# Kernel tuning notes

Hardware: AMD Instinct MI355X
Metric: run time of the kernel (lower is better)

## Reference

```python
import jax, jax.numpy as jnp
import numpy as np

B, L, C, R = 64, 4096, 256, 8
H = C // R  # 32

def setup_inputs() -> dict:
    key = jax.random.key(0)
    k0, k1, k2 = jax.random.split(key, 3)
    inputs = jax.random.normal(k0, (B, L, C), dtype=jnp.float32)
    # Dense weights (glorot-ish scale)
    w1 = jax.random.normal(k1, (C, H), dtype=jnp.float32) * (1.0 / np.sqrt(C))
    b1 = jnp.zeros((H,), dtype=jnp.float32)
    w2 = jax.random.normal(k2, (H, C), dtype=jnp.float32) * (1.0 / np.sqrt(H))
    b2 = jnp.zeros((C,), dtype=jnp.float32)
    return {"inputs": inputs, "w1": w1, "b1": b1, "w2": w2, "b2": b2}

def reference(inputs, w1, b1, w2, b2):
    # squeeze: global average pool over sequence dim -> [B, C]
    s = jnp.mean(inputs, axis=1)
    # excitation: C -> C//R (relu) -> C (sigmoid)
    e = jax.nn.relu(s @ w1 + b1)
    g = jax.nn.sigmoid(e @ w2 + b2)  # [B, C]
    # broadcast gate over sequence dim and scale
    return inputs * g[:, None, :]
```

## Files before the change

kernel.cpp:

```cpp
#include <hip/hip_runtime.h>
#include <math.h>

constexpr int B = 64;
constexpr int L = 4096;
constexpr int C = 256;
constexpr int H = 32;

constexpr int NCHUNK = 32;
constexpr int ROWS = L / NCHUNK;

typedef float v4f __attribute__((ext_vector_type(4)));

__global__ __launch_bounds__(256) void se_reduce(const float* __restrict__ in,
                                                 float* __restrict__ partial) {
    const int b = blockIdx.x / NCHUNK;
    const int chunk = blockIdx.x % NCHUNK;
    const int t = threadIdx.x;
    const int c4 = t & 63;
    const int r0 = t >> 6;

    const v4f* base = reinterpret_cast<const v4f*>(
        in + (size_t)b * L * C + (size_t)chunk * ROWS * C);

    v4f acc = (v4f)(0.f);
    for (int r = r0; r < ROWS; r += 4) {
        acc += base[(size_t)r * (C / 4) + c4];
    }

    __shared__ v4f red[4][C / 4];
    red[r0][c4] = acc;
    __syncthreads();
    if (r0 == 0) {
        v4f s = red[0][c4] + red[1][c4] + red[2][c4] + red[3][c4];
        reinterpret_cast<v4f*>(partial + (size_t)blockIdx.x * C)[c4] = s;
    }
}

__global__ __launch_bounds__(256) void se_gate(const float* __restrict__ partial,
                                               const float* __restrict__ w1,
                                               const float* __restrict__ b1,
                                               const float* __restrict__ w2,
                                               const float* __restrict__ b2,
                                               float* __restrict__ g) {
    const int b = blockIdx.x;
    const int t = threadIdx.x;

    __shared__ float sm[C];
    __shared__ float em[H];

    float acc = 0.f;
    const float* p = partial + (size_t)b * NCHUNK * C + t;
    #pragma unroll 8
    for (int k = 0; k < NCHUNK; ++k) acc += p[(size_t)k * C];
    sm[t] = acc * (1.0f / (float)L);
    __syncthreads();

    if (t < H) {
        float a1 = b1[t];
        #pragma unroll 8
        for (int c = 0; c < C; ++c) a1 += sm[c] * w1[c * H + t];
        em[t] = fmaxf(a1, 0.0f);
    }
    __syncthreads();

    float a2 = b2[t];
    #pragma unroll
    for (int h = 0; h < H; ++h) a2 += em[h] * w2[h * C + t];
    g[b * C + t] = 1.0f / (1.0f + expf(-a2));
}

constexpr size_t TOT4 = (size_t)B * L * C / 4;
constexpr int SCALE_BLOCKS = 2048;
constexpr int SCALE_THREADS = 256;

__global__ __launch_bounds__(256) void se_scale(const v4f* __restrict__ in,
                                                const float* __restrict__ g,
                                                v4f* __restrict__ out) {
    const size_t stride = (size_t)SCALE_BLOCKS * SCALE_THREADS;
    const size_t nsteps = TOT4 / stride;
    const size_t tid = (size_t)blockIdx.x * SCALE_THREADS + threadIdx.x;
    const v4f* g4 = reinterpret_cast<const v4f*>(g);

    for (size_t k = nsteps; k-- > 0;) {
        const size_t i = k * stride + tid;
        v4f v = in[i];
        const size_t b = i >> 18;
        const int c4 = (int)(i & (C / 4 - 1));
        const v4f gv = g4[b * (C / 4) + c4];
        v *= gv;
        __builtin_nontemporal_store(v, &out[i]);
    }
}

extern "C" void kernel_launch(void* const* d_in, const int* in_sizes, int n_in,
                              void* d_out, int out_size, void* d_ws, size_t ws_size,
                              hipStream_t stream) {
    const float* in = (const float*)d_in[0];
    const float* w1 = (const float*)d_in[1];
    const float* b1 = (const float*)d_in[2];
    const float* w2 = (const float*)d_in[3];
    const float* b2 = (const float*)d_in[4];
    float* out = (float*)d_out;

    float* partial = (float*)d_ws;
    float* g = partial + (size_t)B * NCHUNK * C;

    se_reduce<<<B * NCHUNK, 256, 0, stream>>>(in, partial);
    se_gate<<<B, 256, 0, stream>>>(partial, w1, b1, w2, b2, g);
    se_scale<<<SCALE_BLOCKS, SCALE_THREADS, 0, stream>>>(
        reinterpret_cast<const v4f*>(in), g, reinterpret_cast<v4f*>(out));
}
```

Measured before the change: 147.9 us.

## Segment batch into two passes so scale rereads input from cache

Splits the reduce, gate and scale pipeline into two batch segments, launching all three kernels per segment. Each segment's input is small enough that the scale pass can re-read it from the last-level cache right after the reduce pass streamed it, instead of going back to HBM. The scale kernel is also rewritten to use the same chunked block mapping as reduce, with loop unrolling added. This adds extra kernel launches and serialization of the small gate kernel between segments.

```diff
diff --git a/kernel.cpp b/kernel.cpp
--- a/kernel.cpp
+++ b/kernel.cpp
@@ -6,15 +6,18 @@
 constexpr int C = 256;
 constexpr int H = 32;
 
-constexpr int NCHUNK = 32;
-constexpr int ROWS = L / NCHUNK;
+constexpr int NSEG = 2;
+constexpr int BSEG = B / NSEG;
+constexpr int NCH = 32;
+constexpr int ROWS = L / NCH;
 
 typedef float v4f __attribute__((ext_vector_type(4)));
 
 __global__ __launch_bounds__(256) void se_reduce(const float* __restrict__ in,
-                                                 float* __restrict__ partial) {
-    const int b = blockIdx.x / NCHUNK;
-    const int chunk = blockIdx.x % NCHUNK;
+                                                 float* __restrict__ partial,
+                                                 int b0) {
+    const int b = b0 + blockIdx.x / NCH;
+    const int chunk = blockIdx.x % NCH;
     const int t = threadIdx.x;
     const int c4 = t & 63;
     const int r0 = t >> 6;
@@ -23,6 +26,7 @@
         in + (size_t)b * L * C + (size_t)chunk * ROWS * C);
 
     v4f acc = (v4f)(0.f);
+    #pragma unroll 8
     for (int r = r0; r < ROWS; r += 4) {
         acc += base[(size_t)r * (C / 4) + c4];
     }
@@ -32,7 +36,7 @@
     __syncthreads();
     if (r0 == 0) {
         v4f s = red[0][c4] + red[1][c4] + red[2][c4] + red[3][c4];
-        reinterpret_cast<v4f*>(partial + (size_t)blockIdx.x * C)[c4] = s;
+        reinterpret_cast<v4f*>(partial + ((size_t)b * NCH + chunk) * C)[c4] = s;
     }
 }
 
@@ -41,17 +45,18 @@
                                                const float* __restrict__ b1,
                                                const float* __restrict__ w2,
                                                const float* __restrict__ b2,
-                                               float* __restrict__ g) {
-    const int b = blockIdx.x;
+                                               float* __restrict__ g,
+                                               int b0) {
+    const int b = b0 + blockIdx.x;
     const int t = threadIdx.x;
 
     __shared__ float sm[C];
     __shared__ float em[H];
 
     float acc = 0.f;
-    const float* p = partial + (size_t)b * NCHUNK * C + t;
+    const float* p = partial + (size_t)b * NCH * C + t;
     #pragma unroll 8
-    for (int k = 0; k < NCHUNK; ++k) acc += p[(size_t)k * C];
+    for (int k = 0; k < NCH; ++k) acc += p[(size_t)k * C];
     sm[t] = acc * (1.0f / (float)L);
     __syncthreads();
 
@@ -69,25 +74,23 @@
     g[b * C + t] = 1.0f / (1.0f + expf(-a2));
 }
 
-constexpr size_t TOT4 = (size_t)B * L * C / 4;
-constexpr int SCALE_BLOCKS = 2048;
-constexpr int SCALE_THREADS = 256;
-
 __global__ __launch_bounds__(256) void se_scale(const v4f* __restrict__ in,
                                                 const float* __restrict__ g,
-                                                v4f* __restrict__ out) {
-    const size_t stride = (size_t)SCALE_BLOCKS * SCALE_THREADS;
-    const size_t nsteps = TOT4 / stride;
-    const size_t tid = (size_t)blockIdx.x * SCALE_THREADS + threadIdx.x;
-    const v4f* g4 = reinterpret_cast<const v4f*>(g);
+                                                v4f* __restrict__ out,
+                                                int b0) {
+    const int b = b0 + blockIdx.x / NCH;
+    const int chunk = blockIdx.x % NCH;
+    const int t = threadIdx.x;
+    const int c4 = t & 63;
+    const int r0 = t >> 6;
 
-    for (size_t k = nsteps; k-- > 0;) {
-        const size_t i = k * stride + tid;
-        v4f v = in[i];
-        const size_t b = i >> 18;
-        const int c4 = (int)(i & (C / 4 - 1));
-        const v4f gv = g4[b * (C / 4) + c4];
-        v *= gv;
+    const size_t base = (size_t)b * L * (C / 4) + (size_t)chunk * ROWS * (C / 4);
+    const v4f gv = reinterpret_cast<const v4f*>(g)[b * (C / 4) + c4];
+
+    #pragma unroll 8
+    for (int r = r0; r < ROWS; r += 4) {
+        const size_t i = base + (size_t)r * (C / 4) + c4;
+        v4f v = in[i] * gv;
         __builtin_nontemporal_store(v, &out[i]);
     }
 }
@@ -103,10 +106,13 @@
     float* out = (float*)d_out;
 
     float* partial = (float*)d_ws;
-    float* g = partial + (size_t)B * NCHUNK * C;
+    float* g = partial + (size_t)B * NCH * C;
 
-    se_reduce<<<B * NCHUNK, 256, 0, stream>>>(in, partial);
-    se_gate<<<B, 256, 0, stream>>>(partial, w1, b1, w2, b2, g);
-    se_scale<<<SCALE_BLOCKS, SCALE_THREADS, 0, stream>>>(
-        reinterpret_cast<const v4f*>(in), g, reinterpret_cast<v4f*>(out));
+    for (int s = 0; s < NSEG; ++s) {
+        const int b0 = s * BSEG;
+        se_reduce<<<BSEG * NCH, 256, 0, stream>>>(in, partial, b0);
+        se_gate<<<BSEG, 256, 0, stream>>>(partial, w1, b1, w2, b2, g, b0);
+        se_scale<<<BSEG * NCH, 256, 0, stream>>>(
+            reinterpret_cast<const v4f*>(in), g, reinterpret_cast<v4f*>(out), b0);
+    }
 }
```

New measurement: 149.8 us. About the same (+1.3%).
